# Performance work log

Measured on AMD Instinct MI355X. Metric: run time of the kernel, lower is better.

Reference implementation:

```python
import math
import jax, jax.numpy as jnp
import numpy as np

N_INPUT = 256
N_HIDDEN = 512
T = 1024
B = 64
DT = 0.1  # brainstate default environ dt


def setup_inputs() -> dict:
    key = jax.random.key(0)
    k1, k2, k3 = jax.random.split(key, 3)
    inputs = jax.random.normal(k1, (T, B, N_INPUT), dtype=jnp.float32)
    # KaimingNormal: std = sqrt(2 / fan_in)
    W_ih = jax.random.normal(k2, (N_INPUT, N_HIDDEN), dtype=jnp.float32) * math.sqrt(2.0 / N_INPUT)
    b_ih = jnp.zeros((N_HIDDEN,), dtype=jnp.float32)
    W_hh = jax.random.normal(k3, (N_HIDDEN, N_HIDDEN), dtype=jnp.float32) * math.sqrt(2.0 / N_HIDDEN)
    b_hh = jnp.zeros((N_HIDDEN,), dtype=jnp.float32)
    alpha = jnp.full((N_HIDDEN,), 0.04, dtype=jnp.float32)
    omega = jnp.full((N_HIDDEN,), 2.0 * math.pi / 28.0, dtype=jnp.float32)
    gamma = jnp.full((N_HIDDEN,), 0.01, dtype=jnp.float32)
    v = jnp.zeros((N_HIDDEN,), dtype=jnp.float32)
    return dict(inputs=inputs, W_ih=W_ih, b_ih=b_ih, W_hh=W_hh, b_hh=b_hh,
                alpha=alpha, omega=omega, gamma=gamma, v=v)


def reference(inputs, W_ih, b_ih, W_hh, b_hh, alpha, omega, gamma, v):
    n_hidden = W_hh.shape[0]
    gain_rec = 1.0 / math.sqrt(n_hidden)
    h = jnp.float32(DT)
    # external input for the whole sequence: [T, B, H]
    ext = jnp.einsum('tbi,ih->tbh', inputs, W_ih) + b_ih
    om2 = omega * omega          # omega^2
    g2 = 2.0 * gamma             # 2*gamma
    Tt, Bb = ext.shape[0], ext.shape[1]
    x0 = jnp.zeros((Bb, n_hidden), dtype=ext.dtype)
    y0 = jnp.zeros((Bb, n_hidden), dtype=ext.dtype)

    def step(carry, e):
        x, y = carry
        rec = y @ W_hh + b_hh                      # h2h(y)
        inp = e + gain_rec * (rec + v * x)
        y_t = y + h * (alpha * jnp.tanh(inp) - om2 * x - g2 * y)
        x_t = x + h * y_t
        return (x_t, y_t), x_t

    _, out = jax.lax.scan(step, (x0, y0), ext)     # out: [T, B, H]
    return out
```

## Files before the change

### kernel.cpp

```cpp
#include <hip/hip_runtime.h>
#include <math.h>

#define T_STEPS 1024
#define NB 64
#define NH 512
#define NI 256

#define NGRP 4
#define BPG 16
#define WGS_PER_GRP 4

#define WS_YBUF_OFF 4096
#define WS_INIT_BYTES (WS_YBUF_OFF + NB*NH*2)

typedef short short8 __attribute__((ext_vector_type(8)));
typedef float f32x4 __attribute__((ext_vector_type(4)));

__device__ __forceinline__ unsigned short f32_to_bf16(float x) {
    unsigned u = __float_as_uint(x);
    u += 0x7FFFu + ((u >> 16) & 1u);
    return (unsigned short)(u >> 16);
}

__device__ __forceinline__ float tanh_fast(float x) {
    x = fminf(15.f, fmaxf(-15.f, x));
    const float ex = __expf(-2.f * x);
    return __fdividef(1.f - ex, 1.f + ex);
}

__global__ __launch_bounds__(256) void ext_gemm_kernel(
    const float* __restrict__ inputs, const float* __restrict__ W_ih,
    const float* __restrict__ b_ih, float* __restrict__ out)
{
    __shared__ float Wt[NI * 64];
    const int tid    = threadIdx.x;
    const int hgrp   = blockIdx.x & 7;
    const int rowgrp = blockIdx.x >> 3;
    const int hbase  = hgrp * 64;
    const long rowbase = (long)rowgrp * 512;

    for (int idx = tid; idx < NI * 64; idx += 256) {
        int i  = idx >> 6;
        int hh = idx & 63;
        Wt[idx] = W_ih[(size_t)i * NH + hbase + hh];
    }
    const int hq = tid & 15;
    const int r  = tid >> 4;
    const float4 bias = *(const float4*)&b_ih[hbase + hq * 4];
    __syncthreads();

    for (int rc = 0; rc < 32; ++rc) {
        const long row = rowbase + rc * 16 + r;
        const float* __restrict__ inrow = inputs + row * NI;
        float ax = 0.f, ay = 0.f, az = 0.f, aw = 0.f;
        #pragma unroll 4
        for (int i = 0; i < NI; i += 4) {
            const float4 a  = *(const float4*)(inrow + i);
            const float4 w0 = *(const float4*)&Wt[(i + 0) * 64 + hq * 4];
            const float4 w1 = *(const float4*)&Wt[(i + 1) * 64 + hq * 4];
            const float4 w2 = *(const float4*)&Wt[(i + 2) * 64 + hq * 4];
            const float4 w3 = *(const float4*)&Wt[(i + 3) * 64 + hq * 4];
            ax += a.x * w0.x + a.y * w1.x + a.z * w2.x + a.w * w3.x;
            ay += a.x * w0.y + a.y * w1.y + a.z * w2.y + a.w * w3.y;
            az += a.x * w0.z + a.y * w1.z + a.z * w2.z + a.w * w3.z;
            aw += a.x * w0.w + a.y * w1.w + a.z * w2.w + a.w * w3.w;
        }
        float4 o = make_float4(ax + bias.x, ay + bias.y, az + bias.z, aw + bias.w);
        *(float4*)&out[row * NH + hbase + hq * 4] = o;
    }
}

__global__ __launch_bounds__(512, 1) void horn_recurrent_kernel(
    const float* __restrict__ W_hh, const float* __restrict__ b_hh,
    const float* __restrict__ alpha, const float* __restrict__ omega,
    const float* __restrict__ gamma, const float* __restrict__ v,
    float* __restrict__ out, unsigned short* __restrict__ ybuf,
    unsigned* __restrict__ flags)
{
    const int tid  = threadIdx.x;
    const int wave = tid >> 6;
    const int lane = tid & 63;
    const int g    = lane >> 4;
    const int c    = lane & 15;

    const int grp   = blockIdx.x & (NGRP - 1);
    const int wgi   = blockIdx.x >> 2;
    const int bbase = grp * BPG;
    const int h     = wgi * 128 + wave * 16 + c;

    short8 w0, w1, w2, w3, w4, w5, w6, w7, w8, w9, w10, w11, w12, w13, w14, w15;
#define LDW(KB)                                                              \
    {                                                                        \
        const float* wp = W_hh + (size_t)(KB * 32 + 8 * g) * NH + h;         \
        short8 f;                                                            \
        f[0] = (short)f32_to_bf16(wp[0 * NH]);                               \
        f[1] = (short)f32_to_bf16(wp[1 * NH]);                               \
        f[2] = (short)f32_to_bf16(wp[2 * NH]);                               \
        f[3] = (short)f32_to_bf16(wp[3 * NH]);                               \
        f[4] = (short)f32_to_bf16(wp[4 * NH]);                               \
        f[5] = (short)f32_to_bf16(wp[5 * NH]);                               \
        f[6] = (short)f32_to_bf16(wp[6 * NH]);                               \
        f[7] = (short)f32_to_bf16(wp[7 * NH]);                               \
        w##KB = f;                                                           \
    }
    LDW(0)  LDW(1)  LDW(2)  LDW(3)  LDW(4)  LDW(5)  LDW(6)  LDW(7)
    LDW(8)  LDW(9)  LDW(10) LDW(11) LDW(12) LDW(13) LDW(14) LDW(15)
#undef LDW

    const float bhh_r = b_hh[h];
    const float al_r  = alpha[h];
    const float omv   = omega[h];
    const float om2_r = omv * omv;
    const float g2_r  = 2.0f * gamma[h];
    const float v_r   = v[h];
    const float gain  = 0.04419417382415922f;
    const float hdt   = 0.1f;

    float x0 = 0.f, x1 = 0.f, x2 = 0.f, x3 = 0.f;
    float y0 = 0.f, y1 = 0.f, y2 = 0.f, y3 = 0.f;
    float e0, e1, e2, e3;

    {
        const float* ep = out + (size_t)(bbase + 4 * g) * NH + h;
        e0 = ep[0 * NH]; e1 = ep[1 * NH]; e2 = ep[2 * NH]; e3 = ep[3 * NH];
    }

    for (int t = 0; t < T_STEPS; ++t) {
        const unsigned short* __restrict__ ysrc =
            ybuf + (size_t)(t & 1) * NB * NH + (size_t)(bbase + c) * NH + 8 * g;
        f32x4 ac0 = {0.f, 0.f, 0.f, 0.f};
        f32x4 ac1 = ac0, ac2 = ac0, ac3 = ac0;
#define MF(KB, AC)                                                           \
        AC = __builtin_amdgcn_mfma_f32_16x16x32_bf16(                        \
            *(const short8*)(ysrc + KB * 32), w##KB, AC, 0, 0, 0);
        MF(0, ac0)  MF(1, ac1)  MF(2, ac2)  MF(3, ac3)
        MF(4, ac0)  MF(5, ac1)  MF(6, ac2)  MF(7, ac3)
        MF(8, ac0)  MF(9, ac1)  MF(10, ac2) MF(11, ac3)
        MF(12, ac0) MF(13, ac1) MF(14, ac2) MF(15, ac3)
#undef MF
        const f32x4 recv = (ac0 + ac1) + (ac2 + ac3);

#define UPD(R, XR, YR, ER)                                                   \
        {                                                                    \
            const float rec = recv[R] + bhh_r;                               \
            const float inp = ER + gain * (rec + v_r * XR);                  \
            const float yt  = YR + hdt * (al_r * tanh_fast(inp)              \
                                          - om2_r * XR - g2_r * YR);         \
            XR = XR + hdt * yt;                                              \
            YR = yt;                                                         \
        }
        UPD(0, x0, y0, e0) UPD(1, x1, y1, e1) UPD(2, x2, y2, e2) UPD(3, x3, y3, e3)
#undef UPD

        const size_t obase = ((size_t)t * NB + bbase + 4 * g) * NH + h;

        if (t == T_STEPS - 1) {
            out[obase + 0 * NH] = x0; out[obase + 1 * NH] = x1;
            out[obase + 2 * NH] = x2; out[obase + 3 * NH] = x3;
            break;
        }

        {
            unsigned short* ydst = ybuf + (size_t)((t + 1) & 1) * NB * NH
                                        + (size_t)(bbase + 4 * g) * NH + h;
            __hip_atomic_store(ydst + 0 * NH, f32_to_bf16(y0),
                               __ATOMIC_RELAXED, __HIP_MEMORY_SCOPE_AGENT);
            __hip_atomic_store(ydst + 1 * NH, f32_to_bf16(y1),
                               __ATOMIC_RELAXED, __HIP_MEMORY_SCOPE_AGENT);
            __hip_atomic_store(ydst + 2 * NH, f32_to_bf16(y2),
                               __ATOMIC_RELAXED, __HIP_MEMORY_SCOPE_AGENT);
            __hip_atomic_store(ydst + 3 * NH, f32_to_bf16(y3),
                               __ATOMIC_RELAXED, __HIP_MEMORY_SCOPE_AGENT);
        }

        asm volatile("s_waitcnt vmcnt(0)" ::: "memory");
        __syncthreads();
        const unsigned tgt = (unsigned)(t + 1);
        if (tid == 0)
            __hip_atomic_store(flags + grp * 64 + wgi, tgt,
                               __ATOMIC_RELEASE, __HIP_MEMORY_SCOPE_AGENT);

        out[obase + 0 * NH] = x0; out[obase + 1 * NH] = x1;
        out[obase + 2 * NH] = x2; out[obase + 3 * NH] = x3;
        e0 = out[obase + (size_t)NB * NH + 0 * NH];
        e1 = out[obase + (size_t)NB * NH + 1 * NH];
        e2 = out[obase + (size_t)NB * NH + 2 * NH];
        e3 = out[obase + (size_t)NB * NH + 3 * NH];

        if (tid == 0) {
            unsigned* fl = flags + grp * 64;
            for (;;) {
                const unsigned f0 = __hip_atomic_load(fl + 0, __ATOMIC_RELAXED, __HIP_MEMORY_SCOPE_AGENT);
                const unsigned f1 = __hip_atomic_load(fl + 1, __ATOMIC_RELAXED, __HIP_MEMORY_SCOPE_AGENT);
                const unsigned f2 = __hip_atomic_load(fl + 2, __ATOMIC_RELAXED, __HIP_MEMORY_SCOPE_AGENT);
                const unsigned f3 = __hip_atomic_load(fl + 3, __ATOMIC_RELAXED, __HIP_MEMORY_SCOPE_AGENT);
                if (f0 >= tgt && f1 >= tgt && f2 >= tgt && f3 >= tgt) break;
                __builtin_amdgcn_s_sleep(2);
            }
            __builtin_amdgcn_fence(__ATOMIC_ACQUIRE, "agent");
        }
        __syncthreads();
    }
}

extern "C" void kernel_launch(void* const* d_in, const int* in_sizes, int n_in,
                              void* d_out, int out_size, void* d_ws, size_t ws_size,
                              hipStream_t stream) {
    const float* inputs = (const float*)d_in[0];
    const float* W_ih   = (const float*)d_in[1];
    const float* b_ih   = (const float*)d_in[2];
    const float* W_hh   = (const float*)d_in[3];
    const float* b_hh   = (const float*)d_in[4];
    const float* alpha  = (const float*)d_in[5];
    const float* omega  = (const float*)d_in[6];
    const float* gamma  = (const float*)d_in[7];
    const float* v      = (const float*)d_in[8];
    float* out = (float*)d_out;

    unsigned* flags      = (unsigned*)d_ws;
    unsigned short* ybuf = (unsigned short*)((char*)d_ws + WS_YBUF_OFF);

    hipMemsetAsync(d_ws, 0, WS_INIT_BYTES, stream);

    ext_gemm_kernel<<<dim3(1024), dim3(256), 0, stream>>>(inputs, W_ih, b_ih, out);

    horn_recurrent_kernel<<<dim3(NGRP * WGS_PER_GRP), dim3(512), 0, stream>>>(
        W_hh, b_hh, alpha, omega, gamma, v, out, ybuf, flags);
}
```

Before: 6.152 ms.

## Stage W_hh in LDS, load y via atomic loads, relax flag fences and polling

New measurement: 9.172 ms. 1.49x slower.

```diff
diff --git a/kernel.cpp b/kernel.cpp
--- a/kernel.cpp
+++ b/kernel.cpp
@@ -15,6 +15,7 @@
 
 typedef short short8 __attribute__((ext_vector_type(8)));
 typedef float f32x4 __attribute__((ext_vector_type(4)));
+typedef unsigned long long u64x2 __attribute__((ext_vector_type(2)));
 
 __device__ __forceinline__ unsigned short f32_to_bf16(float x) {
     unsigned u = __float_as_uint(x);
@@ -77,6 +78,8 @@
     float* __restrict__ out, unsigned short* __restrict__ ybuf,
     unsigned* __restrict__ flags)
 {
+    __shared__ short8 Wf[8][16][64];
+
     const int tid  = threadIdx.x;
     const int wave = tid >> 6;
     const int lane = tid & 63;
@@ -88,24 +91,14 @@
     const int bbase = grp * BPG;
     const int h     = wgi * 128 + wave * 16 + c;
 
-    short8 w0, w1, w2, w3, w4, w5, w6, w7, w8, w9, w10, w11, w12, w13, w14, w15;
-#define LDW(KB)                                                              \
-    {                                                                        \
-        const float* wp = W_hh + (size_t)(KB * 32 + 8 * g) * NH + h;         \
-        short8 f;                                                            \
-        f[0] = (short)f32_to_bf16(wp[0 * NH]);                               \
-        f[1] = (short)f32_to_bf16(wp[1 * NH]);                               \
-        f[2] = (short)f32_to_bf16(wp[2 * NH]);                               \
-        f[3] = (short)f32_to_bf16(wp[3 * NH]);                               \
-        f[4] = (short)f32_to_bf16(wp[4 * NH]);                               \
-        f[5] = (short)f32_to_bf16(wp[5 * NH]);                               \
-        f[6] = (short)f32_to_bf16(wp[6 * NH]);                               \
-        f[7] = (short)f32_to_bf16(wp[7 * NH]);                               \
-        w##KB = f;                                                           \
-    }
-    LDW(0)  LDW(1)  LDW(2)  LDW(3)  LDW(4)  LDW(5)  LDW(6)  LDW(7)
-    LDW(8)  LDW(9)  LDW(10) LDW(11) LDW(12) LDW(13) LDW(14) LDW(15)
-#undef LDW
+    for (int kb = 0; kb < 16; ++kb) {
+        const float* wp = W_hh + (size_t)(kb * 32 + 8 * g) * NH + h;
+        short8 f;
+        #pragma unroll
+        for (int j = 0; j < 8; ++j)
+            f[j] = (short)f32_to_bf16(wp[(size_t)j * NH]);
+        Wf[wave][kb][lane] = f;
+    }
 
     const float bhh_r = b_hh[h];
     const float al_r  = alpha[h];
@@ -124,15 +117,27 @@
         const float* ep = out + (size_t)(bbase + 4 * g) * NH + h;
         e0 = ep[0 * NH]; e1 = ep[1 * NH]; e2 = ep[2 * NH]; e3 = ep[3 * NH];
     }
+    __syncthreads();
 
     for (int t = 0; t < T_STEPS; ++t) {
-        const unsigned short* __restrict__ ysrc =
-            ybuf + (size_t)(t & 1) * NB * NH + (size_t)(bbase + c) * NH + 8 * g;
+        const unsigned long long* __restrict__ ysrc = (const unsigned long long*)
+            (ybuf + (size_t)(t & 1) * NB * NH + (size_t)(bbase + c) * NH + 8 * g);
+#define LDA(KB) \
+        const unsigned long long a##KB##_0 = __hip_atomic_load(ysrc + KB * 8 + 0, __ATOMIC_RELAXED, __HIP_MEMORY_SCOPE_AGENT); \
+        const unsigned long long a##KB##_1 = __hip_atomic_load(ysrc + KB * 8 + 1, __ATOMIC_RELAXED, __HIP_MEMORY_SCOPE_AGENT);
+        LDA(0)  LDA(1)  LDA(2)  LDA(3)  LDA(4)  LDA(5)  LDA(6)  LDA(7)
+        LDA(8)  LDA(9)  LDA(10) LDA(11) LDA(12) LDA(13) LDA(14) LDA(15)
+#undef LDA
+
         f32x4 ac0 = {0.f, 0.f, 0.f, 0.f};
         f32x4 ac1 = ac0, ac2 = ac0, ac3 = ac0;
 #define MF(KB, AC)                                                           \
-        AC = __builtin_amdgcn_mfma_f32_16x16x32_bf16(                        \
-            *(const short8*)(ysrc + KB * 32), w##KB, AC, 0, 0, 0);
+        {                                                                    \
+            u64x2 p; p.x = a##KB##_0; p.y = a##KB##_1;                       \
+            const short8 af = __builtin_bit_cast(short8, p);                 \
+            AC = __builtin_amdgcn_mfma_f32_16x16x32_bf16(                    \
+                af, Wf[wave][KB][lane], AC, 0, 0, 0);                        \
+        }
         MF(0, ac0)  MF(1, ac1)  MF(2, ac2)  MF(3, ac3)
         MF(4, ac0)  MF(5, ac1)  MF(6, ac2)  MF(7, ac3)
         MF(8, ac0)  MF(9, ac1)  MF(10, ac2) MF(11, ac3)
@@ -178,7 +183,7 @@
         const unsigned tgt = (unsigned)(t + 1);
         if (tid == 0)
             __hip_atomic_store(flags + grp * 64 + wgi, tgt,
-                               __ATOMIC_RELEASE, __HIP_MEMORY_SCOPE_AGENT);
+                               __ATOMIC_RELAXED, __HIP_MEMORY_SCOPE_AGENT);
 
         out[obase + 0 * NH] = x0; out[obase + 1 * NH] = x1;
         out[obase + 2 * NH] = x2; out[obase + 3 * NH] = x3;
@@ -188,16 +193,17 @@
         e3 = out[obase + (size_t)NB * NH + 3 * NH];
 
         if (tid == 0) {
-            unsigned* fl = flags + grp * 64;
+            const unsigned long long* fl =
+                (const unsigned long long*)(flags + grp * 64);
             for (;;) {
-                const unsigned f0 = __hip_atomic_load(fl + 0, __ATOMIC_RELAXED, __HIP_MEMORY_SCOPE_AGENT);
-                const unsigned f1 = __hip_atomic_load(fl + 1, __ATOMIC_RELAXED, __HIP_MEMORY_SCOPE_AGENT);
-                const unsigned f2 = __hip_atomic_load(fl + 2, __ATOMIC_RELAXED, __HIP_MEMORY_SCOPE_AGENT);
-                const unsigned f3 = __hip_atomic_load(fl + 3, __ATOMIC_RELAXED, __HIP_MEMORY_SCOPE_AGENT);
-                if (f0 >= tgt && f1 >= tgt && f2 >= tgt && f3 >= tgt) break;
-                __builtin_amdgcn_s_sleep(2);
+                const unsigned long long f01 =
+                    __hip_atomic_load(fl + 0, __ATOMIC_RELAXED, __HIP_MEMORY_SCOPE_AGENT);
+                const unsigned long long f23 =
+                    __hip_atomic_load(fl + 1, __ATOMIC_RELAXED, __HIP_MEMORY_SCOPE_AGENT);
+                if ((unsigned)f01 >= tgt && (unsigned)(f01 >> 32) >= tgt &&
+                    (unsigned)f23 >= tgt && (unsigned)(f23 >> 32) >= tgt) break;
+                __builtin_amdgcn_s_sleep(1);
             }
-            __builtin_amdgcn_fence(__ATOMIC_ACQUIRE, "agent");
         }
         __syncthreads();
     }
```
